# Performance work log

Measured on AMD Instinct MI355X. Metric: run time of the kernel, lower is better.

## Reference

```python
import jax, jax.numpy as jnp
import numpy as np

KH, KW = 3, 3
SH, SW = 1, 1


def _extract_patches(x, kh, kw, sh, sw):
    # x: (B,H,W,C) channels_last -> (B,oR,oC,kh*kw*C), flattened in (kh,kw,C)
    # order to match Keras' reshape of inputs[:, slice_row, slice_col, :].
    B, H, W, C = x.shape
    oR = (H - kh) // sh + 1
    oC = (W - kw) // sw + 1
    cols = []
    for di in range(kh):
        for dj in range(kw):
            cols.append(x[:, di:di + oR * sh:sh, dj:dj + oC * sw:sw, :])
    patches = jnp.stack(cols, axis=3)  # (B,oR,oC,kh*kw,C)
    return patches.reshape(B, oR, oC, kh * kw * C), oR, oC


def setup_inputs() -> dict:
    key = jax.random.key(0)
    k1, k2, k3 = jax.random.split(key, 3)
    B, H, W, C = 64, 32, 32, 64
    filters = 64
    oR = (H - KH) // SH + 1  # 30
    oC = (W - KW) // SW + 1  # 30
    feat = KH * KW * C       # 576
    x = jax.random.normal(k1, (B, H, W, C), dtype=jnp.float32)
    # glorot-ish scaling on the per-location kernel
    kernel = jax.random.normal(k2, (oR * oC, feat, filters), dtype=jnp.float32) * (1.0 / np.sqrt(feat))
    bias = jax.random.normal(k3, (oR, oC, filters), dtype=jnp.float32) * 0.02
    return {"x": x, "kernel": kernel, "bias": bias}


def reference(x, kernel, bias):
    B = x.shape[0]
    patches, oR, oC = _extract_patches(x, KH, KW, SH, SW)  # (B,oR,oC,F)
    feat = patches.shape[-1]
    patches = patches.reshape(B, oR * oC, feat)             # (B,P,F)
    # per-location matmul with unshared weights: (B,P,F) x (P,F,O) -> (B,P,O)
    out = jnp.einsum('bpf,pfo->bpo', patches, kernel)
    out = out.reshape(B, oR, oC, kernel.shape[-1]) + bias[None]
    return jax.nn.relu(out)
```

## Files before the change

kernel.cpp:

```cpp
#include <hip/hip_runtime.h>
#include <hip/hip_bf16.h>

typedef __attribute__((ext_vector_type(4))) float  f32x4;
typedef __attribute__((ext_vector_type(4))) float  float4v;
typedef __attribute__((ext_vector_type(8))) short  bf16x8;
typedef __attribute__((ext_vector_type(4))) short  bf16x4;

#define LDT     72
#define XSTR_B  65536
#define XSTR_H  2048
#define XSTR_W  64
#define WSTR_P  36864
#define OSTR_B  57600

__device__ __forceinline__ short f2bf(float f) {
  union { float f; unsigned u; } v; v.f = f;
  unsigned r = v.u + 0x7fffu + ((v.u >> 16) & 1u);
  return (short)(r >> 16);
}

__global__ __launch_bounds__(256, 2)
void lc2d_kernel(const float* __restrict__ x, const float* __restrict__ wgt,
                 const float* __restrict__ bias, float* __restrict__ out) {
  __shared__ short Asm[64 * LDT];
  __shared__ short Wsm[64 * LDT];

  int orig = blockIdx.x;
  int xcd  = orig & 7;
  int idx  = orig >> 3;
  int p = (xcd < 4 ? xcd * 113 : 4 * 113 + (xcd - 4) * 112) + idx;
  int r = p / 30;
  int c = p - r * 30;

  int tid  = threadIdx.x;
  int lane = tid & 63;
  int wid  = tid >> 6;
  int wr   = (wid >> 1) * 32;
  int wc   = (wid & 1) * 32;
  int l16  = lane & 15;
  int lhi  = lane >> 4;

  int ac4   = (tid & 15) * 4;
  int arow0 = tid >> 4;

  const float* xbase = x + (r * XSTR_H + c * XSTR_W);
  const float* wbase = wgt + p * WSTR_P;

  float4v av[2][4];
  float   wv[2][16];

  f32x4 acc[2][2] = {{{0.f,0.f,0.f,0.f},{0.f,0.f,0.f,0.f}},
                     {{0.f,0.f,0.f,0.f},{0.f,0.f,0.f,0.f}}};

  const float* bb = bias + (r * 30 + c) * 64;
  float bv0 = bb[wc + l16];
  float bv1 = bb[wc + 16 + l16];

  auto issue_loads = [&](int t, int pb) {
    int di = t / 3, dj = t - di * 3;
    const float* xa = xbase + di * XSTR_H + dj * XSTR_W + ac4;
#pragma unroll
    for (int it = 0; it < 4; ++it) {
      int b = it * 16 + arow0;
      av[pb][it] = *(const float4v*)(xa + (long)b * XSTR_B);
    }
    const float* wa = wbase + (t * 64 + wid * 16) * 64 + lane;
#pragma unroll
    for (int i = 0; i < 16; ++i) wv[pb][i] = __builtin_nontemporal_load(wa + i * 64);
  };

  issue_loads(0, 0);
  issue_loads(1, 1);

#pragma unroll
  for (int t = 0; t < 9; ++t) {
    const int pb = t & 1;
    __syncthreads();
#pragma unroll
    for (int it = 0; it < 4; ++it) {
      int b = it * 16 + arow0;
      bf16x4 w4 = { f2bf(av[pb][it].x), f2bf(av[pb][it].y), f2bf(av[pb][it].z), f2bf(av[pb][it].w) };
      *(bf16x4*)&Asm[b * LDT + ac4] = w4;
    }
    {
      bf16x8 lo, hi;
#pragma unroll
      for (int i = 0; i < 8; ++i) { lo[i] = f2bf(wv[pb][i]); hi[i] = f2bf(wv[pb][8 + i]); }
      *(bf16x8*)&Wsm[lane * LDT + wid * 16]     = lo;
      *(bf16x8*)&Wsm[lane * LDT + wid * 16 + 8] = hi;
    }
    if (t < 7) issue_loads(t + 2, pb);
    __syncthreads();
#pragma unroll
    for (int s = 0; s < 2; ++s) {
      int kb = s * 32 + lhi * 8;
      bf16x8 a0 = *(const bf16x8*)&Asm[(wr +  0 + l16) * LDT + kb];
      bf16x8 a1 = *(const bf16x8*)&Asm[(wr + 16 + l16) * LDT + kb];
      bf16x8 b0 = *(const bf16x8*)&Wsm[(wc +  0 + l16) * LDT + kb];
      bf16x8 b1 = *(const bf16x8*)&Wsm[(wc + 16 + l16) * LDT + kb];
      acc[0][0] = __builtin_amdgcn_mfma_f32_16x16x32_bf16(a0, b0, acc[0][0], 0, 0, 0);
      acc[0][1] = __builtin_amdgcn_mfma_f32_16x16x32_bf16(a0, b1, acc[0][1], 0, 0, 0);
      acc[1][0] = __builtin_amdgcn_mfma_f32_16x16x32_bf16(a1, b0, acc[1][0], 0, 0, 0);
      acc[1][1] = __builtin_amdgcn_mfma_f32_16x16x32_bf16(a1, b1, acc[1][1], 0, 0, 0);
    }
  }

  float* ob = out + (r * 30 + c) * 64;
#pragma unroll
  for (int m = 0; m < 2; ++m) {
#pragma unroll
    for (int j = 0; j < 4; ++j) {
      int b = wr + m * 16 + lhi * 4 + j;
#pragma unroll
      for (int n = 0; n < 2; ++n) {
        float v = acc[m][n][j] + (n ? bv1 : bv0);
        __builtin_nontemporal_store(fmaxf(v, 0.f), &ob[(long)b * OSTR_B + wc + n * 16 + l16]);
      }
    }
  }
}

extern "C" void kernel_launch(void* const* d_in, const int* in_sizes, int n_in,
                              void* d_out, int out_size, void* d_ws, size_t ws_size,
                              hipStream_t stream) {
  const float* x    = (const float*)d_in[0];
  const float* wgt  = (const float*)d_in[1];
  const float* bias = (const float*)d_in[2];
  float* out = (float*)d_out;
  hipLaunchKernelGGL(lc2d_kernel, dim3(900), dim3(256), 0, stream, x, wgt, bias, out);
}
```

Before: 205.0 us.

## Give each wave private LDS tiles and drop block-wide barriers

```diff
diff --git a/kernel.cpp b/kernel.cpp
--- a/kernel.cpp
+++ b/kernel.cpp
@@ -1,12 +1,12 @@
 #include <hip/hip_runtime.h>
 #include <hip/hip_bf16.h>
 
+typedef __attribute__((ext_vector_type(4))) float  float4v;
 typedef __attribute__((ext_vector_type(4))) float  f32x4;
-typedef __attribute__((ext_vector_type(4))) float  float4v;
 typedef __attribute__((ext_vector_type(8))) short  bf16x8;
 typedef __attribute__((ext_vector_type(4))) short  bf16x4;
 
-#define LDT     72
+#define LDK     40
 #define XSTR_B  65536
 #define XSTR_H  2048
 #define XSTR_W  64
@@ -18,106 +18,95 @@
   unsigned r = v.u + 0x7fffu + ((v.u >> 16) & 1u);
   return (short)(r >> 16);
 }
+__device__ __forceinline__ bf16x4 cvt4(float4v v) {
+  bf16x4 o; o[0] = f2bf(v.x); o[1] = f2bf(v.y); o[2] = f2bf(v.z); o[3] = f2bf(v.w);
+  return o;
+}
 
 __global__ __launch_bounds__(256, 2)
 void lc2d_kernel(const float* __restrict__ x, const float* __restrict__ wgt,
                  const float* __restrict__ bias, float* __restrict__ out) {
-  __shared__ short Asm[64 * LDT];
-  __shared__ short Wsm[64 * LDT];
+  __shared__ short Xs[4 * 2 * 64 * LDK];
+  __shared__ short Ws[4 * 2 * 16 * LDK];
 
   int orig = blockIdx.x;
   int xcd  = orig & 7;
   int idx  = orig >> 3;
-  int p = (xcd < 4 ? xcd * 113 : 4 * 113 + (xcd - 4) * 112) + idx;
+  int p = (xcd < 4 ? xcd * 113 : 452 + (xcd - 4) * 112) + idx;
   int r = p / 30;
   int c = p - r * 30;
 
   int tid  = threadIdx.x;
   int lane = tid & 63;
   int wid  = tid >> 6;
-  int wr   = (wid >> 1) * 32;
-  int wc   = (wid & 1) * 32;
   int l16  = lane & 15;
   int lhi  = lane >> 4;
 
-  int ac4   = (tid & 15) * 4;
-  int arow0 = tid >> 4;
+  int bx  = lane >> 3;
+  int kx0 = (lane & 7) * 4;
+  int krs = lane >> 2;
+  int wo0 = (lane & 3) * 4;
 
-  const float* xbase = x + (r * XSTR_H + c * XSTR_W);
-  const float* wbase = wgt + p * WSTR_P;
+  short* Xw = Xs + wid * (2 * 64 * LDK);
+  short* Ww = Ws + wid * (2 * 16 * LDK);
 
-  float4v av[2][4];
-  float   wv[2][16];
+  const float* xbase = x + r * XSTR_H + c * XSTR_W + kx0;
+  const float* wbase = wgt + p * WSTR_P + wid * 16 + wo0;
 
-  f32x4 acc[2][2] = {{{0.f,0.f,0.f,0.f},{0.f,0.f,0.f,0.f}},
-                     {{0.f,0.f,0.f,0.f},{0.f,0.f,0.f,0.f}}};
+  float4v xv[2][8];
+  float4v wv[2][2];
+  f32x4 acc[4] = {{0.f,0.f,0.f,0.f},{0.f,0.f,0.f,0.f},{0.f,0.f,0.f,0.f},{0.f,0.f,0.f,0.f}};
 
-  const float* bb = bias + (r * 30 + c) * 64;
-  float bv0 = bb[wc + l16];
-  float bv1 = bb[wc + 16 + l16];
+  const float bval = bias[(r * 30 + c) * 64 + wid * 16 + l16];
 
-  auto issue_loads = [&](int t, int pb) {
-    int di = t / 3, dj = t - di * 3;
-    const float* xa = xbase + di * XSTR_H + dj * XSTR_W + ac4;
+  auto issue = [&](int t, int pb) {
+    int tap = t >> 1, di = tap / 3, dj = tap - di * 3;
+    const float* xa = xbase + di * XSTR_H + dj * XSTR_W + (t & 1) * 32;
 #pragma unroll
-    for (int it = 0; it < 4; ++it) {
-      int b = it * 16 + arow0;
-      av[pb][it] = *(const float4v*)(xa + (long)b * XSTR_B);
-    }
-    const float* wa = wbase + (t * 64 + wid * 16) * 64 + lane;
+    for (int i = 0; i < 8; ++i)
+      xv[pb][i] = *(const float4v*)(xa + (long)(i * 8 + bx) * XSTR_B);
+    const float* wa = wbase + t * 32 * 64;
 #pragma unroll
-    for (int i = 0; i < 16; ++i) wv[pb][i] = __builtin_nontemporal_load(wa + i * 64);
+    for (int i = 0; i < 2; ++i)
+      wv[pb][i] = *(const float4v*)(wa + (i * 16 + krs) * 64);
   };
 
-  issue_loads(0, 0);
-  issue_loads(1, 1);
+  issue(0, 0);
+  issue(1, 1);
 
 #pragma unroll
-  for (int t = 0; t < 9; ++t) {
+  for (int t = 0; t < 18; ++t) {
     const int pb = t & 1;
-    __syncthreads();
+    short* Xb = Xw + pb * (64 * LDK);
+    short* Wb = Ww + pb * (16 * LDK);
 #pragma unroll
-    for (int it = 0; it < 4; ++it) {
-      int b = it * 16 + arow0;
-      bf16x4 w4 = { f2bf(av[pb][it].x), f2bf(av[pb][it].y), f2bf(av[pb][it].z), f2bf(av[pb][it].w) };
-      *(bf16x4*)&Asm[b * LDT + ac4] = w4;
+    for (int i = 0; i < 8; ++i)
+      *(bf16x4*)&Xb[(i * 8 + bx) * LDK + kx0] = cvt4(xv[pb][i]);
+#pragma unroll
+    for (int i = 0; i < 2; ++i) {
+      int kr = i * 16 + krs;
+      Wb[(wo0 + 0) * LDK + kr] = f2bf(wv[pb][i].x);
+      Wb[(wo0 + 1) * LDK + kr] = f2bf(wv[pb][i].y);
+      Wb[(wo0 + 2) * LDK + kr] = f2bf(wv[pb][i].z);
+      Wb[(wo0 + 3) * LDK + kr] = f2bf(wv[pb][i].w);
     }
-    {
-      bf16x8 lo, hi;
+    if (t < 16) issue(t + 2, pb);
+    bf16x8 bf = *(const bf16x8*)&Wb[l16 * LDK + lhi * 8];
 #pragma unroll
-      for (int i = 0; i < 8; ++i) { lo[i] = f2bf(wv[pb][i]); hi[i] = f2bf(wv[pb][8 + i]); }
-      *(bf16x8*)&Wsm[lane * LDT + wid * 16]     = lo;
-      *(bf16x8*)&Wsm[lane * LDT + wid * 16 + 8] = hi;
-    }
-    if (t < 7) issue_loads(t + 2, pb);
-    __syncthreads();
-#pragma unroll
-    for (int s = 0; s < 2; ++s) {
-      int kb = s * 32 + lhi * 8;
-      bf16x8 a0 = *(const bf16x8*)&Asm[(wr +  0 + l16) * LDT + kb];
-      bf16x8 a1 = *(const bf16x8*)&Asm[(wr + 16 + l16) * LDT + kb];
-      bf16x8 b0 = *(const bf16x8*)&Wsm[(wc +  0 + l16) * LDT + kb];
-      bf16x8 b1 = *(const bf16x8*)&Wsm[(wc + 16 + l16) * LDT + kb];
-      acc[0][0] = __builtin_amdgcn_mfma_f32_16x16x32_bf16(a0, b0, acc[0][0], 0, 0, 0);
-      acc[0][1] = __builtin_amdgcn_mfma_f32_16x16x32_bf16(a0, b1, acc[0][1], 0, 0, 0);
-      acc[1][0] = __builtin_amdgcn_mfma_f32_16x16x32_bf16(a1, b0, acc[1][0], 0, 0, 0);
-      acc[1][1] = __builtin_amdgcn_mfma_f32_16x16x32_bf16(a1, b1, acc[1][1], 0, 0, 0);
+    for (int m = 0; m < 4; ++m) {
+      bf16x8 af = *(const bf16x8*)&Xb[(m * 16 + l16) * LDK + lhi * 8];
+      acc[m] = __builtin_amdgcn_mfma_f32_16x16x32_bf16(af, bf, acc[m], 0, 0, 0);
     }
   }
 
-  float* ob = out + (r * 30 + c) * 64;
+  float* ob = out + (r * 30 + c) * 64 + wid * 16 + l16;
 #pragma unroll
-  for (int m = 0; m < 2; ++m) {
+  for (int m = 0; m < 4; ++m)
 #pragma unroll
     for (int j = 0; j < 4; ++j) {
-      int b = wr + m * 16 + lhi * 4 + j;
-#pragma unroll
-      for (int n = 0; n < 2; ++n) {
-        float v = acc[m][n][j] + (n ? bv1 : bv0);
-        __builtin_nontemporal_store(fmaxf(v, 0.f), &ob[(long)b * OSTR_B + wc + n * 16 + l16]);
-      }
+      int b = m * 16 + lhi * 4 + j;
+      ob[(long)b * OSTR_B] = fmaxf(acc[m][j] + bval, 0.f);
     }
-  }
 }
 
 extern "C" void kernel_launch(void* const* d_in, const int* in_sizes, int n_in,
```

After: 218.6 us. +6.6%, slower.
